# Kernel tuning notes

Hardware: AMD Instinct MI355X
Metric: run time of the kernel (lower is better)

Reference implementation:

```python
import jax, jax.numpy as jnp
import numpy as np

B, C, H, W = 4, 128, 256, 256
HIDDEN = max(C // 8, 4)  # SE hidden


def haar_dwt(x):
    # x: (B,C,H,W), H,W even. Haar 2x2 stride-2 depthwise conv via block reshape.
    b_, c_, h_, w_ = x.shape
    xb = x.reshape(b_, c_, h_ // 2, 2, w_ // 2, 2)
    a = xb[:, :, :, 0, :, 0]
    b = xb[:, :, :, 0, :, 1]
    c = xb[:, :, :, 1, :, 0]
    d = xb[:, :, :, 1, :, 1]
    LL = 0.5 * (a + b + c + d)
    LH = 0.5 * (-a + b - c + d)
    HL = 0.5 * (-a - b + c + d)
    HH = 0.5 * (a - b - c + d)
    return LH, HL, HH, LL


def haar_idwt(LH, HL, HH, LL):
    # inverse of the depthwise conv_transpose with the same Haar kernels
    a = 0.5 * (LL - LH - HL + HH)
    b = 0.5 * (LL + LH - HL - HH)
    c = 0.5 * (LL - LH + HL - HH)
    d = 0.5 * (LL + LH + HL + HH)
    top = jnp.stack([a, b], axis=-1)      # (B,C,h,w,2)
    bot = jnp.stack([c, d], axis=-1)      # (B,C,h,w,2)
    blk = jnp.stack([top, bot], axis=-2)  # (B,C,h,w,2,2) -> rows x cols
    Bs, Cs, h, w = LL.shape
    return blk.transpose(0, 1, 2, 4, 3, 5).reshape(Bs, Cs, 2 * h, 2 * w)


def soft_threshold(x, thr):
    return jnp.sign(x) * jax.nn.relu(jnp.abs(x) - thr)


def setup_inputs() -> dict:
    key = jax.random.key(0)
    ks = jax.random.split(key, 9)
    x = jax.random.normal(ks[0], (B, C, H, W), dtype=jnp.float32)
    theta = jax.random.normal(ks[1], (3, C, 1, 1), dtype=jnp.float32) * 0.02
    dir_gate = jax.random.normal(ks[2], (3, C, 1, 1), dtype=jnp.float32) * 0.02
    fc_w = jax.random.normal(ks[3], (C, C), dtype=jnp.float32) * (1.0 / np.sqrt(C))
    fc_b = jax.random.normal(ks[4], (C,), dtype=jnp.float32) * 0.02
    sub_redistribute = jax.random.normal(ks[5], (C, 3), dtype=jnp.float32) * 0.02
    se_w1 = jax.random.normal(ks[6], (HIDDEN, C), dtype=jnp.float32) * (1.0 / np.sqrt(C))
    se_b1 = jnp.zeros((HIDDEN,), dtype=jnp.float32)
    se_w2 = jax.random.normal(ks[7], (C, HIDDEN), dtype=jnp.float32) * (1.0 / np.sqrt(HIDDEN))
    se_b2 = jnp.zeros((C,), dtype=jnp.float32)
    gamma = jnp.float32(0.5)
    return {"x": x, "theta": theta, "dir_gate": dir_gate, "fc_w": fc_w,
            "fc_b": fc_b, "sub_redistribute": sub_redistribute,
            "se_w1": se_w1, "se_b1": se_b1, "se_w2": se_w2, "se_b2": se_b2,
            "gamma": gamma}


def reference(x, theta, dir_gate, fc_w, fc_b, sub_redistribute,
              se_w1, se_b1, se_w2, se_b2, gamma):
    eps = 1e-6
    LH, HL, HH, LL = haar_dwt(x)

    # per-(B,C) abs-mean thresholds
    m_LH = jnp.mean(jnp.abs(LH), axis=(2, 3), keepdims=True) + eps
    m_HL = jnp.mean(jnp.abs(HL), axis=(2, 3), keepdims=True) + eps
    m_HH = jnp.mean(jnp.abs(HH), axis=(2, 3), keepdims=True) + eps
    t = jax.nn.sigmoid(theta)  # (3,C,1,1)
    LH_hat = soft_threshold(LH, t[0][None] * m_LH)
    HL_hat = soft_threshold(HL, t[1][None] * m_HL)
    HH_hat = soft_threshold(HH, t[2][None] * m_HH)

    g = jax.nn.sigmoid(dir_gate)
    LH_hat = LH_hat * g[0][None]
    HL_hat = HL_hat * g[1][None]
    HH_hat = HH_hat * g[2][None]

    stack3 = jnp.stack([LH_hat, HL_hat, HH_hat], axis=2)  # (B,C,3,h,w)
    attn_band = jax.nn.softmax(jnp.mean(jnp.abs(stack3), axis=1, keepdims=True), axis=2)
    H_mix = jnp.sum(stack3 * attn_band, axis=2)  # (B,C,h,w)

    w_redis = jax.nn.softmax(sub_redistribute, axis=1)  # (C,3)
    H_redist = H_mix[:, :, None] * w_redis[None, :, :, None, None]  # (B,C,3,h,w)
    X_re = haar_idwt(H_redist[:, :, 0], H_redist[:, :, 1], H_redist[:, :, 2], LL)

    # channel softmax gate from GAP + fc
    gap_vec = jnp.mean(X_re, axis=(2, 3))  # (B,C)
    gap_vec = gap_vec @ fc_w.T + fc_b
    w_softmax = jax.nn.softmax(gap_vec, axis=1)[:, :, None, None]

    # SE gate
    z = jnp.mean(X_re, axis=(2, 3))  # (B,C)
    z = jax.nn.relu(z @ se_w1.T + se_b1)
    w_se = jax.nn.sigmoid(z @ se_w2.T + se_b2)[:, :, None, None]

    return x * w_softmax + gamma * (X_re * w_se)
```

## Files before the change

### kernel.cpp

```cpp
#include <hip/hip_runtime.h>
#include <math.h>

#define BB 4
#define CC 128
#define HHH 256
#define WWW 256
#define HWSZ (HHH*WWW)
#define HIDDEN 16
#define NPAIR 8192
#define FP 8
#define NFCHUNK (NPAIR/FP)
#define NG 32
#define RQUART 4
#define CPW 17

typedef float nfloat4 __attribute__((ext_vector_type(4)));

struct CParams {
    float thr0, thr1, thr2;
    float gA0, gA1, gA2;
    float gF0, gF1, gF2;
    float wsm, e0q;
    float ca, cb, cc, cd;
    float pad0;
};
static_assert(sizeof(CParams) == 64, "CParams must be 64B");

__device__ __forceinline__ float sigmoidf_(float v) { return 1.0f / (1.0f + expf(-v)); }

__global__ __launch_bounds__(256) void k_reduce(const float* __restrict__ x,
                                                float4* __restrict__ partial) {
    const int bq = blockIdx.x;
    const int bc = bq >> 2;
    const int quarter = bq & 3;
    const float* base = x + (size_t)bc * HWSZ;
    const int tid = threadIdx.x;
    float a0 = 0.f, a1 = 0.f, a2 = 0.f, sx = 0.f;
    #pragma unroll
    for (int i = 0; i < 8; ++i) {
        const int p = quarter * 2048 + i * 256 + tid;
        const int r = p >> 6;
        const int q = p & 63;
        const float4 t  = *(const float4*)(base + (2*r)   * WWW + 4*q);
        const float4 bo = *(const float4*)(base + (2*r+1) * WWW + 4*q);
        {   const float a = t.x, b_ = t.y, c_ = bo.x, d = bo.y;
            const float u1 = a + b_, u2 = c_ + d, u3 = a + c_, u4 = b_ + d, u5 = a + d, u6 = b_ + c_;
            a0 += fabsf(u4 - u3);
            a1 += fabsf(u2 - u1);
            a2 += fabsf(u5 - u6);
            sx += u1 + u2;
        }
        {   const float a = t.z, b_ = t.w, c_ = bo.z, d = bo.w;
            const float u1 = a + b_, u2 = c_ + d, u3 = a + c_, u4 = b_ + d, u5 = a + d, u6 = b_ + c_;
            a0 += fabsf(u4 - u3);
            a1 += fabsf(u2 - u1);
            a2 += fabsf(u5 - u6);
            sx += u1 + u2;
        }
    }
    __shared__ float4 red[256];
    red[tid] = make_float4(a0, a1, a2, sx);
    __syncthreads();
    for (int off = 128; off > 0; off >>= 1) {
        if (tid < off) {
            float4 o = red[tid + off];
            red[tid].x += o.x; red[tid].y += o.y; red[tid].z += o.z; red[tid].w += o.w;
        }
        __syncthreads();
    }
    if (tid == 0) partial[bq] = red[0];
}

__global__ __launch_bounds__(128) void k_params(
    const float4* __restrict__ partial,
    const float* __restrict__ theta, const float* __restrict__ dir_gate,
    const float* __restrict__ fc_w, const float* __restrict__ fc_b,
    const float* __restrict__ sub_r,
    const float* __restrict__ se_w1, const float* __restrict__ se_b1,
    const float* __restrict__ se_w2, const float* __restrict__ se_b2,
    const float* __restrict__ gamma_p,
    CParams* __restrict__ cbuf)
{
    const int b = blockIdx.x;
    const int i = threadIdx.x;
    __shared__ float gap[CC];
    __shared__ float z1[HIDDEN];
    __shared__ float red[CC];

    float4 s = make_float4(0.f, 0.f, 0.f, 0.f);
    #pragma unroll
    for (int k = 0; k < RQUART; ++k) {
        const float4 pq = partial[(b * CC + i) * RQUART + k];
        s.x += pq.x; s.y += pq.y; s.z += pq.z; s.w += pq.w;
    }
    gap[i] = s.w * (1.0f / 65536.0f);
    __syncthreads();

    float y = fc_b[i];
    for (int j = 0; j < CC; ++j) y += gap[j] * fc_w[i * CC + j];
    if (i < HIDDEN) {
        float z = se_b1[i];
        for (int j = 0; j < CC; ++j) z += gap[j] * se_w1[i * CC + j];
        z1[i] = fmaxf(z, 0.0f);
    }
    red[i] = y;
    __syncthreads();
    float mx = -1e30f;
    for (int j = 0; j < CC; ++j) mx = fmaxf(mx, red[j]);
    const float e = expf(y - mx);
    __syncthreads();
    red[i] = e;
    __syncthreads();
    float ssum = 0.f;
    for (int j = 0; j < CC; ++j) ssum += red[j];
    const float wsm = e / ssum;

    float wse = se_b2[i];
    for (int h = 0; h < HIDDEN; ++h) wse += z1[h] * se_w2[i * HIDDEN + h];
    wse = sigmoidf_(wse);
    const float wse2 = gamma_p[0] * wse;

    const float m0 = s.x * (0.5f / 16384.0f) + 1e-6f;
    const float m1 = s.y * (0.5f / 16384.0f) + 1e-6f;
    const float m2 = s.z * (0.5f / 16384.0f) + 1e-6f;
    CParams p;
    const float g0 = sigmoidf_(dir_gate[0 * CC + i]);
    const float g1 = sigmoidf_(dir_gate[1 * CC + i]);
    const float g2 = sigmoidf_(dir_gate[2 * CC + i]);
    p.thr0 = 2.0f * sigmoidf_(theta[0 * CC + i]) * m0;
    p.thr1 = 2.0f * sigmoidf_(theta[1 * CC + i]) * m1;
    p.thr2 = 2.0f * sigmoidf_(theta[2 * CC + i]) * m2;
    p.gA0 = g0; p.gA1 = g1; p.gA2 = g2;
    p.gF0 = 0.5f * g0 * wse2;
    p.gF1 = 0.5f * g1 * wse2;
    p.gF2 = 0.5f * g2 * wse2;
    p.wsm = wsm;
    p.e0q = 0.25f * wse2;
    const float r0 = sub_r[i * 3 + 0], r1 = sub_r[i * 3 + 1], r2 = sub_r[i * 3 + 2];
    const float rm = fmaxf(r0, fmaxf(r1, r2));
    const float e0 = expf(r0 - rm), e1 = expf(r1 - rm), e2 = expf(r2 - rm);
    const float inv = 1.0f / (e0 + e1 + e2);
    const float w0 = e0 * inv, w1 = e1 * inv, w2 = e2 * inv;
    p.ca = 0.5f * (-w0 - w1 + w2);
    p.cb = 0.5f * ( w0 - w1 - w2);
    p.cc = 0.5f * (-w0 + w1 - w2);
    p.cd = 0.5f * ( w0 + w1 + w2);
    p.pad0 = 0.f;
    cbuf[b * CC + i] = p;
}

__global__ __launch_bounds__(256) void k_fused(const float* __restrict__ x,
                                               const CParams* __restrict__ cbuf,
                                               float* __restrict__ out) {
    const int b = blockIdx.y;
    const int chunk = blockIdx.x;
    const int tid = threadIdx.x;
    const int pp = tid & 7;
    const int g  = tid >> 3;

    __shared__ float cpa[CC * CPW];
    __shared__ float red2[NG][FP][6];
    __shared__ float vsum[FP][6];
    __shared__ float att2[FP][4];
    {
        const float* src = (const float*)(cbuf + b * CC);
        for (int i = tid; i < CC * 16; i += 256) {
            const int c = i >> 4, f = i & 15;
            cpa[c * CPW + f] = src[i];
        }
    }
    __syncthreads();

    const int p  = chunk * FP + pp;
    const int rp = p >> 6, q = p & 63;
    const float* base = x + (size_t)b * CC * HWSZ + (2*rp) * WWW + 4*q;

    float4 st[4], sb[4];
    float sA0=0, sA1=0, sA2=0, sB0=0, sB1=0, sB2=0;
    #pragma unroll
    for (int ci = 0; ci < 4; ++ci) {
        const int c = g * 4 + ci;
        const float* pc = base + c * HWSZ;
        st[ci] = *(const float4*)(pc);
        sb[ci] = *(const float4*)(pc + WWW);
        const float* cp = cpa + c * CPW;
        const float thr0 = cp[0], thr1 = cp[1], thr2 = cp[2];
        const float gA0 = cp[3], gA1 = cp[4], gA2 = cp[5];
        {   const float a = st[ci].x, b_ = st[ci].y, c_ = sb[ci].x, d = sb[ci].y;
            const float u1 = a + b_, u2 = c_ + d, u3 = a + c_, u4 = b_ + d, u5 = a + d, u6 = b_ + c_;
            sA0 += gA0 * fmaxf(fabsf(u4 - u3) - thr0, 0.f);
            sA1 += gA1 * fmaxf(fabsf(u2 - u1) - thr1, 0.f);
            sA2 += gA2 * fmaxf(fabsf(u5 - u6) - thr2, 0.f);
        }
        {   const float a = st[ci].z, b_ = st[ci].w, c_ = sb[ci].z, d = sb[ci].w;
            const float u1 = a + b_, u2 = c_ + d, u3 = a + c_, u4 = b_ + d, u5 = a + d, u6 = b_ + c_;
            sB0 += gA0 * fmaxf(fabsf(u4 - u3) - thr0, 0.f);
            sB1 += gA1 * fmaxf(fabsf(u2 - u1) - thr1, 0.f);
            sB2 += gA2 * fmaxf(fabsf(u5 - u6) - thr2, 0.f);
        }
    }
    red2[g][pp][0] = sA0; red2[g][pp][1] = sA1; red2[g][pp][2] = sA2;
    red2[g][pp][3] = sB0; red2[g][pp][4] = sB1; red2[g][pp][5] = sB2;
    __syncthreads();

    if (tid < FP * 6) {
        const int pair = tid & 7, kk = tid >> 3;
        float acc = 0.f;
        #pragma unroll
        for (int gg = 0; gg < NG; ++gg) acc += red2[gg][pair][kk];
        vsum[pair][kk] = acc;
    }
    __syncthreads();
    if (tid < FP * 2) {
        const int pair = tid >> 1, h = tid & 1;
        const float v0 = vsum[pair][3*h+0] * (0.5f / CC);
        const float v1 = vsum[pair][3*h+1] * (0.5f / CC);
        const float v2 = vsum[pair][3*h+2] * (0.5f / CC);
        const float mx = fmaxf(v0, fmaxf(v1, v2));
        const float e0 = expf(v0 - mx), e1 = expf(v1 - mx), e2 = expf(v2 - mx);
        const float inv = 1.0f / (e0 + e1 + e2);
        att2[pair][2*h + 0] = e0 * inv;
        att2[pair][2*h + 1] = e1 * inv;
    }
    __syncthreads();

    const float a0A = att2[pp][0], a1A = att2[pp][1], a2A = 1.0f - a0A - a1A;
    const float a0B = att2[pp][2], a1B = att2[pp][3], a2B = 1.0f - a0B - a1B;

    float* obase = out + (size_t)b * CC * HWSZ + (2*rp) * WWW + 4*q;
    #pragma unroll
    for (int ci = 0; ci < 4; ++ci) {
        const int c = g * 4 + ci;
        const float* cp = cpa + c * CPW;
        const float thr0 = cp[0], thr1 = cp[1], thr2 = cp[2];
        const float gF0 = cp[6], gF1 = cp[7], gF2 = cp[8];
        const float wsm = cp[9], e0q = cp[10];
        const float ca = cp[11], cb = cp[12], ccc = cp[13], cd = cp[14];
        const float m0A = a0A * gF0, m1A = a1A * gF1, m2A = a2A * gF2;
        const float m0B = a0B * gF0, m1B = a1B * gF1, m2B = a2B * gF2;
        nfloat4 otop, obot;
        {   const float a = st[ci].x, b_ = st[ci].y, c_ = sb[ci].x, d = sb[ci].y;
            const float u1 = a + b_, u2 = c_ + d, u3 = a + c_, u4 = b_ + d, u5 = a + d, u6 = b_ + c_;
            const float B0 = u4 - u3, B1 = u2 - u1, B2 = u5 - u6;
            const float LL2 = u1 + u2;
            const float s0 = copysignf(fmaxf(fabsf(B0) - thr0, 0.f), B0);
            const float s1 = copysignf(fmaxf(fabsf(B1) - thr1, 0.f), B1);
            const float s2 = copysignf(fmaxf(fabsf(B2) - thr2, 0.f), B2);
            const float Hf = s0*m0A + s1*m1A + s2*m2A;
            const float T  = e0q * LL2;
            otop.x = fmaf(a , wsm, fmaf(Hf, ca , T));
            otop.y = fmaf(b_, wsm, fmaf(Hf, cb , T));
            obot.x = fmaf(c_, wsm, fmaf(Hf, ccc, T));
            obot.y = fmaf(d , wsm, fmaf(Hf, cd , T));
        }
        {   const float a = st[ci].z, b_ = st[ci].w, c_ = sb[ci].z, d = sb[ci].w;
            const float u1 = a + b_, u2 = c_ + d, u3 = a + c_, u4 = b_ + d, u5 = a + d, u6 = b_ + c_;
            const float B0 = u4 - u3, B1 = u2 - u1, B2 = u5 - u6;
            const float LL2 = u1 + u2;
            const float s0 = copysignf(fmaxf(fabsf(B0) - thr0, 0.f), B0);
            const float s1 = copysignf(fmaxf(fabsf(B1) - thr1, 0.f), B1);
            const float s2 = copysignf(fmaxf(fabsf(B2) - thr2, 0.f), B2);
            const float Hf = s0*m0B + s1*m1B + s2*m2B;
            const float T  = e0q * LL2;
            otop.z = fmaf(a , wsm, fmaf(Hf, ca , T));
            otop.w = fmaf(b_, wsm, fmaf(Hf, cb , T));
            obot.z = fmaf(c_, wsm, fmaf(Hf, ccc, T));
            obot.w = fmaf(d , wsm, fmaf(Hf, cd , T));
        }
        float* po = obase + c * HWSZ;
        __builtin_nontemporal_store(otop, (nfloat4*)(po));
        __builtin_nontemporal_store(obot, (nfloat4*)(po + WWW));
    }
}

extern "C" void kernel_launch(void* const* d_in, const int* in_sizes, int n_in,
                              void* d_out, int out_size, void* d_ws, size_t ws_size,
                              hipStream_t stream) {
    const float* x        = (const float*)d_in[0];
    const float* theta    = (const float*)d_in[1];
    const float* dir_gate = (const float*)d_in[2];
    const float* fc_w     = (const float*)d_in[3];
    const float* fc_b     = (const float*)d_in[4];
    const float* sub_r    = (const float*)d_in[5];
    const float* se_w1    = (const float*)d_in[6];
    const float* se_b1    = (const float*)d_in[7];
    const float* se_w2    = (const float*)d_in[8];
    const float* se_b2    = (const float*)d_in[9];
    const float* gamma_p  = (const float*)d_in[10];
    float* out = (float*)d_out;

    char* ws = (char*)d_ws;
    float4*  partial = (float4*)(ws);
    CParams* cbuf    = (CParams*)(ws + 32768);

    k_reduce<<<dim3(BB * CC * RQUART), dim3(256), 0, stream>>>(x, partial);
    k_params<<<dim3(BB), dim3(CC), 0, stream>>>(partial, theta, dir_gate, fc_w, fc_b,
                                                sub_r, se_w1, se_b1, se_w2, se_b2,
                                                gamma_p, cbuf);
    k_fused<<<dim3(NFCHUNK, BB), dim3(256), 0, stream>>>(x, cbuf, out);
}
```

Baseline: 76.27 us.

## Restructure fused kernel into 32-pair tiles with double-buffered LDS channel staging

The fused kernel now processes 32 pixel pairs (a 2-row strip of 128 columns) per 512-thread block. Each thread loads one float4 per channel slice across 16 channel chunks and holds all of them in a register stash, and the rows are exchanged through double-buffered shared memory. The intent is wider, fully coalesced row loads, more work per block and fewer blocks, with the reduction simplified to 8 partials per pair. In exchange there is a __syncthreads per channel chunk in both passes, extra LDS traffic, and 16 float4 of registers per thread at launch_bounds(512,4), which could spill.

```diff
diff --git a/kernel.cpp b/kernel.cpp
--- a/kernel.cpp
+++ b/kernel.cpp
@@ -3,16 +3,15 @@
 
 #define BB 4
 #define CC 128
-#define HHH 256
 #define WWW 256
-#define HWSZ (HHH*WWW)
+#define HWSZ 65536
 #define HIDDEN 16
-#define NPAIR 8192
-#define FP 8
-#define NFCHUNK (NPAIR/FP)
-#define NG 32
 #define RQUART 4
 #define CPW 17
+#define TP 32
+#define NTILE 256
+#define NCH 8
+#define NCHK 16
 
 typedef float nfloat4 __attribute__((ext_vector_type(4)));
 
@@ -149,127 +148,116 @@
     cbuf[b * CC + i] = p;
 }
 
-__global__ __launch_bounds__(256) void k_fused(const float* __restrict__ x,
-                                               const CParams* __restrict__ cbuf,
-                                               float* __restrict__ out) {
+__global__ __launch_bounds__(512, 4) void k_fused(const float* __restrict__ x,
+                                                  const CParams* __restrict__ cbuf,
+                                                  float* __restrict__ out) {
     const int b = blockIdx.y;
-    const int chunk = blockIdx.x;
+    const int tile = blockIdx.x;
     const int tid = threadIdx.x;
-    const int pp = tid & 7;
-    const int g  = tid >> 3;
-
-    __shared__ float cpa[CC * CPW];
-    __shared__ float red2[NG][FP][6];
-    __shared__ float vsum[FP][6];
-    __shared__ float att2[FP][4];
+    const int ch  = tid >> 6;
+    const int h   = (tid >> 5) & 1;
+    const int col = tid & 31;
+    const int o   = tid & 63;
+    const int j   = o & 31;
+    const int e   = o >> 5;
+
+    __shared__ float  cpa[CC * CPW];
+    __shared__ float4 buf[2][NCH][2][TP];
+    __shared__ float  red[NCH][64][3];
+    __shared__ float  att2[64][2];
     {
         const float* src = (const float*)(cbuf + b * CC);
-        for (int i = tid; i < CC * 16; i += 256) {
-            const int c = i >> 4, f = i & 15;
-            cpa[c * CPW + f] = src[i];
-        }
-    }
-    __syncthreads();
-
-    const int p  = chunk * FP + pp;
-    const int rp = p >> 6, q = p & 63;
-    const float* base = x + (size_t)b * CC * HWSZ + (2*rp) * WWW + 4*q;
-
-    float4 st[4], sb[4];
-    float sA0=0, sA1=0, sA2=0, sB0=0, sB1=0, sB2=0;
-    #pragma unroll
-    for (int ci = 0; ci < 4; ++ci) {
-        const int c = g * 4 + ci;
-        const float* pc = base + c * HWSZ;
-        st[ci] = *(const float4*)(pc);
-        sb[ci] = *(const float4*)(pc + WWW);
+        for (int i = tid; i < CC * 16; i += 512) cpa[(i >> 4) * CPW + (i & 15)] = src[i];
+    }
+
+    const int p0 = tile * TP;
+    const int rp = p0 >> 6, q0 = p0 & 63;
+    const size_t base = (size_t)b * CC * HWSZ + (size_t)(2 * rp) * WWW + 4 * q0;
+    const size_t toff = base + (size_t)ch * HWSZ + (size_t)h * WWW + 4 * (size_t)col;
+
+    float4 stash[NCHK];
+    stash[0] = *(const float4*)(x + toff);
+    stash[1] = *(const float4*)(x + toff + (size_t)NCH * HWSZ);
+    buf[0][ch][h][col] = stash[0];
+    __syncthreads();
+
+    float s0 = 0.f, s1 = 0.f, s2 = 0.f;
+    #pragma unroll
+    for (int k = 0; k < NCHK; ++k) {
+        if (k < NCHK - 2) stash[k + 2] = *(const float4*)(x + toff + (size_t)(k + 2) * NCH * HWSZ);
+        if (k < NCHK - 1) buf[(k + 1) & 1][ch][h][col] = stash[k + 1];
+        const int c = k * NCH + ch;
+        const float4 t  = buf[k & 1][ch][0][j];
+        const float4 bo = buf[k & 1][ch][1][j];
+        const float a  = e ? t.z  : t.x,  b_ = e ? t.w  : t.y;
+        const float c_ = e ? bo.z : bo.x, d  = e ? bo.w : bo.y;
+        const float u1 = a + b_, u2 = c_ + d, u3 = a + c_, u4 = b_ + d, u5 = a + d, u6 = b_ + c_;
         const float* cp = cpa + c * CPW;
-        const float thr0 = cp[0], thr1 = cp[1], thr2 = cp[2];
-        const float gA0 = cp[3], gA1 = cp[4], gA2 = cp[5];
-        {   const float a = st[ci].x, b_ = st[ci].y, c_ = sb[ci].x, d = sb[ci].y;
-            const float u1 = a + b_, u2 = c_ + d, u3 = a + c_, u4 = b_ + d, u5 = a + d, u6 = b_ + c_;
-            sA0 += gA0 * fmaxf(fabsf(u4 - u3) - thr0, 0.f);
-            sA1 += gA1 * fmaxf(fabsf(u2 - u1) - thr1, 0.f);
-            sA2 += gA2 * fmaxf(fabsf(u5 - u6) - thr2, 0.f);
-        }
-        {   const float a = st[ci].z, b_ = st[ci].w, c_ = sb[ci].z, d = sb[ci].w;
-            const float u1 = a + b_, u2 = c_ + d, u3 = a + c_, u4 = b_ + d, u5 = a + d, u6 = b_ + c_;
-            sB0 += gA0 * fmaxf(fabsf(u4 - u3) - thr0, 0.f);
-            sB1 += gA1 * fmaxf(fabsf(u2 - u1) - thr1, 0.f);
-            sB2 += gA2 * fmaxf(fabsf(u5 - u6) - thr2, 0.f);
-        }
-    }
-    red2[g][pp][0] = sA0; red2[g][pp][1] = sA1; red2[g][pp][2] = sA2;
-    red2[g][pp][3] = sB0; red2[g][pp][4] = sB1; red2[g][pp][5] = sB2;
-    __syncthreads();
-
-    if (tid < FP * 6) {
-        const int pair = tid & 7, kk = tid >> 3;
-        float acc = 0.f;
+        s0 += cp[3] * fmaxf(fabsf(u4 - u3) - cp[0], 0.f);
+        s1 += cp[4] * fmaxf(fabsf(u2 - u1) - cp[1], 0.f);
+        s2 += cp[5] * fmaxf(fabsf(u5 - u6) - cp[2], 0.f);
+        __syncthreads();
+    }
+    red[ch][o][0] = s0; red[ch][o][1] = s1; red[ch][o][2] = s2;
+    __syncthreads();
+
+    if (tid < 64) {
+        float v0 = 0.f, v1 = 0.f, v2 = 0.f;
         #pragma unroll
-        for (int gg = 0; gg < NG; ++gg) acc += red2[gg][pair][kk];
-        vsum[pair][kk] = acc;
-    }
-    __syncthreads();
-    if (tid < FP * 2) {
-        const int pair = tid >> 1, h = tid & 1;
-        const float v0 = vsum[pair][3*h+0] * (0.5f / CC);
-        const float v1 = vsum[pair][3*h+1] * (0.5f / CC);
-        const float v2 = vsum[pair][3*h+2] * (0.5f / CC);
+        for (int s = 0; s < NCH; ++s) { v0 += red[s][tid][0]; v1 += red[s][tid][1]; v2 += red[s][tid][2]; }
+        v0 *= (0.5f / CC); v1 *= (0.5f / CC); v2 *= (0.5f / CC);
         const float mx = fmaxf(v0, fmaxf(v1, v2));
         const float e0 = expf(v0 - mx), e1 = expf(v1 - mx), e2 = expf(v2 - mx);
         const float inv = 1.0f / (e0 + e1 + e2);
-        att2[pair][2*h + 0] = e0 * inv;
-        att2[pair][2*h + 1] = e1 * inv;
-    }
-    __syncthreads();
-
-    const float a0A = att2[pp][0], a1A = att2[pp][1], a2A = 1.0f - a0A - a1A;
-    const float a0B = att2[pp][2], a1B = att2[pp][3], a2B = 1.0f - a0B - a1B;
-
-    float* obase = out + (size_t)b * CC * HWSZ + (2*rp) * WWW + 4*q;
-    #pragma unroll
-    for (int ci = 0; ci < 4; ++ci) {
-        const int c = g * 4 + ci;
+        att2[tid][0] = e0 * inv; att2[tid][1] = e1 * inv;
+    }
+    __syncthreads();
+
+    const float aA0 = att2[col][0],      aA1 = att2[col][1],      aA2 = 1.0f - aA0 - aA1;
+    const float aB0 = att2[32 + col][0], aB1 = att2[32 + col][1], aB2 = 1.0f - aB0 - aB1;
+    buf[0][ch][h][col] = stash[0];
+    __syncthreads();
+    #pragma unroll
+    for (int k = 0; k < NCHK; ++k) {
+        if (k < NCHK - 1) buf[(k + 1) & 1][ch][h][col] = stash[k + 1];
+        const int c = k * NCH + ch;
+        const float4 t  = buf[k & 1][ch][0][col];
+        const float4 bo = buf[k & 1][ch][1][col];
         const float* cp = cpa + c * CPW;
         const float thr0 = cp[0], thr1 = cp[1], thr2 = cp[2];
         const float gF0 = cp[6], gF1 = cp[7], gF2 = cp[8];
         const float wsm = cp[9], e0q = cp[10];
         const float ca = cp[11], cb = cp[12], ccc = cp[13], cd = cp[14];
-        const float m0A = a0A * gF0, m1A = a1A * gF1, m2A = a2A * gF2;
-        const float m0B = a0B * gF0, m1B = a1B * gF1, m2B = a2B * gF2;
-        nfloat4 otop, obot;
-        {   const float a = st[ci].x, b_ = st[ci].y, c_ = sb[ci].x, d = sb[ci].y;
-            const float u1 = a + b_, u2 = c_ + d, u3 = a + c_, u4 = b_ + d, u5 = a + d, u6 = b_ + c_;
-            const float B0 = u4 - u3, B1 = u2 - u1, B2 = u5 - u6;
-            const float LL2 = u1 + u2;
-            const float s0 = copysignf(fmaxf(fabsf(B0) - thr0, 0.f), B0);
-            const float s1 = copysignf(fmaxf(fabsf(B1) - thr1, 0.f), B1);
-            const float s2 = copysignf(fmaxf(fabsf(B2) - thr2, 0.f), B2);
-            const float Hf = s0*m0A + s1*m1A + s2*m2A;
-            const float T  = e0q * LL2;
-            otop.x = fmaf(a , wsm, fmaf(Hf, ca , T));
-            otop.y = fmaf(b_, wsm, fmaf(Hf, cb , T));
-            obot.x = fmaf(c_, wsm, fmaf(Hf, ccc, T));
-            obot.y = fmaf(d , wsm, fmaf(Hf, cd , T));
-        }
-        {   const float a = st[ci].z, b_ = st[ci].w, c_ = sb[ci].z, d = sb[ci].w;
-            const float u1 = a + b_, u2 = c_ + d, u3 = a + c_, u4 = b_ + d, u5 = a + d, u6 = b_ + c_;
-            const float B0 = u4 - u3, B1 = u2 - u1, B2 = u5 - u6;
-            const float LL2 = u1 + u2;
-            const float s0 = copysignf(fmaxf(fabsf(B0) - thr0, 0.f), B0);
-            const float s1 = copysignf(fmaxf(fabsf(B1) - thr1, 0.f), B1);
-            const float s2 = copysignf(fmaxf(fabsf(B2) - thr2, 0.f), B2);
-            const float Hf = s0*m0B + s1*m1B + s2*m2B;
-            const float T  = e0q * LL2;
-            otop.z = fmaf(a , wsm, fmaf(Hf, ca , T));
-            otop.w = fmaf(b_, wsm, fmaf(Hf, cb , T));
-            obot.z = fmaf(c_, wsm, fmaf(Hf, ccc, T));
-            obot.w = fmaf(d , wsm, fmaf(Hf, cd , T));
-        }
-        float* po = obase + c * HWSZ;
-        __builtin_nontemporal_store(otop, (nfloat4*)(po));
-        __builtin_nontemporal_store(obot, (nfloat4*)(po + WWW));
+        float HfA, TA;
+        {   const float a = t.x, b_ = t.y, c_ = bo.x, d = bo.y;
+            const float u1 = a + b_, u2 = c_ + d, u3 = a + c_, u4 = b_ + d, u5 = a + d, u6 = b_ + c_;
+            const float B0 = u4 - u3, B1 = u2 - u1, B2 = u5 - u6, LL2 = u1 + u2;
+            const float ss0 = copysignf(fmaxf(fabsf(B0) - thr0, 0.f), B0);
+            const float ss1 = copysignf(fmaxf(fabsf(B1) - thr1, 0.f), B1);
+            const float ss2 = copysignf(fmaxf(fabsf(B2) - thr2, 0.f), B2);
+            HfA = ss0 * (aA0 * gF0) + ss1 * (aA1 * gF1) + ss2 * (aA2 * gF2);
+            TA  = e0q * LL2;
+        }
+        float HfB, TB;
+        {   const float a = t.z, b_ = t.w, c_ = bo.z, d = bo.w;
+            const float u1 = a + b_, u2 = c_ + d, u3 = a + c_, u4 = b_ + d, u5 = a + d, u6 = b_ + c_;
+            const float B0 = u4 - u3, B1 = u2 - u1, B2 = u5 - u6, LL2 = u1 + u2;
+            const float ss0 = copysignf(fmaxf(fabsf(B0) - thr0, 0.f), B0);
+            const float ss1 = copysignf(fmaxf(fabsf(B1) - thr1, 0.f), B1);
+            const float ss2 = copysignf(fmaxf(fabsf(B2) - thr2, 0.f), B2);
+            HfB = ss0 * (aB0 * gF0) + ss1 * (aB1 * gF1) + ss2 * (aB2 * gF2);
+            TB  = e0q * LL2;
+        }
+        const float pa = h ? bo.x : t.x, pb = h ? bo.y : t.y;
+        const float pz = h ? bo.z : t.z, pw = h ? bo.w : t.w;
+        const float k1 = h ? ccc : ca,   k2 = h ? cd  : cb;
+        nfloat4 o4;
+        o4.x = fmaf(pa, wsm, fmaf(HfA, k1, TA));
+        o4.y = fmaf(pb, wsm, fmaf(HfA, k2, TA));
+        o4.z = fmaf(pz, wsm, fmaf(HfB, k1, TB));
+        o4.w = fmaf(pw, wsm, fmaf(HfB, k2, TB));
+        __builtin_nontemporal_store(o4, (nfloat4*)(out + toff + (size_t)k * NCH * HWSZ));
+        __syncthreads();
     }
 }
 
@@ -297,5 +285,5 @@
     k_params<<<dim3(BB), dim3(CC), 0, stream>>>(partial, theta, dir_gate, fc_w, fc_b,
                                                 sub_r, se_w1, se_b1, se_w2, se_b2,
                                                 gamma_p, cbuf);
-    k_fused<<<dim3(NFCHUNK, BB), dim3(256), 0, stream>>>(x, cbuf, out);
-}
+    k_fused<<<dim3(NTILE, BB), dim3(512), 0, stream>>>(x, cbuf, out);
+}
```

After: 119.8 us. +57.1%, slower.
